# Optimization experiments

Hardware: AMD Instinct MI355X
Metric: run time of the kernel (lower is better)

## Reference

```python
import jax, jax.numpy as jnp
import numpy as np

VOCAB, EMB, HID, B, S = 32000, 256, 512, 64, 512


def setup_inputs() -> dict:
    key = jax.random.key(0)
    ks = jax.random.split(key, 8)
    sc = 0.05
    return {
        "X": jax.random.randint(ks[0], (B, S), 0, VOCAB, dtype=jnp.int32),
        "emb": jax.random.normal(ks[1], (VOCAB, EMB), jnp.float32) * sc,
        "W_ih": jax.random.normal(ks[2], (HID, EMB), jnp.float32) * sc,
        "W_hh": jax.random.normal(ks[3], (HID, HID), jnp.float32) * sc,
        "b_ih": jax.random.normal(ks[4], (HID,), jnp.float32) * sc,
        "b_hh": jax.random.normal(ks[5], (HID,), jnp.float32) * sc,
        "W": jax.random.normal(ks[6], (VOCAB, 2 * HID), jnp.float32) * sc,
        "b": jnp.ones((VOCAB,), jnp.float32),
    }


def reference(X, emb, W_ih, W_hh, b_ih, b_hh, W, b):
    # Embedding lookup -> [S, B, E] (seq-first, like torch RNN default)
    x = emb[X].transpose(1, 0, 2)
    # Precompute input projections for all steps: [S, B, H]
    xin = jnp.einsum('sbe,he->sbh', x, W_ih) + b_ih + b_hh
    h0 = jnp.zeros((X.shape[0], W_hh.shape[0]), x.dtype)

    def step(h, xt):
        h = jnp.tanh(xt + h @ W_hh.T)
        return h, h

    _, outputs = jax.lax.scan(step, h0, xin)  # [S, B, H]
    last = outputs[-1]                         # [B, H]
    prev = outputs[:-1]                        # [S-1, B, H]
    # Attention scores between each previous step and the last output
    scores = jnp.einsum('sbh,bh->sb', prev, last)      # [S-1, B]
    attn = jax.nn.softmax(scores, axis=0)              # softmax over time
    ctx = jnp.einsum('sb,sbh->bh', attn, prev)         # [B, H]
    feat = jnp.concatenate([ctx, last], axis=1)        # [B, 2H]
    return feat @ W.T + b                              # [B, n_class]
```

## Files before the change

kernel.cpp:

```cpp
#include <hip/hip_runtime.h>
#include <hip/hip_fp16.h>
#include <stdint.h>

#define VOCAB 32000
#define EMB   256
#define HID   512
#define BATCH 64
#define SEQ   512

typedef _Float16 h2_t __attribute__((ext_vector_type(2)));

__device__ __forceinline__ float fdot2(unsigned int a, unsigned int b, float c) {
#if __has_builtin(__builtin_amdgcn_fdot2)
    return __builtin_amdgcn_fdot2(__builtin_bit_cast(h2_t, a),
                                  __builtin_bit_cast(h2_t, b), c, false);
#else
    __half2 ah = __builtin_bit_cast(__half2, a);
    __half2 bh = __builtin_bit_cast(__half2, b);
    float2 af = __half22float2(ah), bf = __half22float2(bh);
    return fmaf(af.y, bf.y, fmaf(af.x, bf.x, c));
#endif
}

template<int CTRL>
__device__ __forceinline__ float quad_add(float x) {
    int v = __builtin_amdgcn_update_dpp(0, __builtin_bit_cast(int, x),
                                        CTRL, 0xF, 0xF, true);
    return x + __builtin_bit_cast(float, v);
}
__device__ __forceinline__ float quad_reduce(float x) {
    x = quad_add<0xB1>(x);
    x = quad_add<0x4E>(x);
    return x;
}

__global__ void prep_whh(const float* __restrict__ W_hh, unsigned int* __restrict__ Wpk) {
    int idx = blockIdx.x * blockDim.x + threadIdx.x;
    if (idx >= HID * (HID / 2)) return;
    int r = idx & (HID - 1);
    int j = idx >> 9;
    float lo = W_hh[r * HID + 2 * j];
    float hi = W_hh[r * HID + 2 * j + 1];
    unsigned int u = ((unsigned int)__half_as_ushort(__float2half(hi)) << 16)
                   |  (unsigned int)__half_as_ushort(__float2half(lo));
    Wpk[idx] = u;
}

#define TSA 132

__global__ __launch_bounds__(256) void embed_gemm(
    const int* __restrict__ X, const float* __restrict__ emb,
    const float* __restrict__ W_ih, const float* __restrict__ b_ih,
    const float* __restrict__ b_hh, __half* __restrict__ xin) {
    __shared__ float A_l[32 * TSA];
    __shared__ float B_l[32 * TSA];
    const int tid = threadIdx.x;
    const int tx = tid & 15, ty = tid >> 4;
    const int sb0 = blockIdx.x * 128;
    const int h0  = blockIdx.y * 128;

    float acc[8][8] = {};

    for (int kc = 0; kc < EMB; kc += 32) {
#pragma unroll
        for (int q = 0; q < 4; ++q) {
            int idx = q * 256 + tid;
            int r  = idx >> 3;
            int c4 = idx & 7;
            int row = X[sb0 + r];
            float4 v = *(const float4*)(emb + (size_t)row * EMB + kc + c4 * 4);
            A_l[(c4 * 4 + 0) * TSA + r] = v.x;
            A_l[(c4 * 4 + 1) * TSA + r] = v.y;
            A_l[(c4 * 4 + 2) * TSA + r] = v.z;
            A_l[(c4 * 4 + 3) * TSA + r] = v.w;
        }
#pragma unroll
        for (int q = 0; q < 4; ++q) {
            int idx = q * 256 + tid;
            int r  = idx >> 3;
            int c4 = idx & 7;
            float4 v = *(const float4*)(W_ih + (size_t)(h0 + r) * EMB + kc + c4 * 4);
            B_l[(c4 * 4 + 0) * TSA + r] = v.x;
            B_l[(c4 * 4 + 1) * TSA + r] = v.y;
            B_l[(c4 * 4 + 2) * TSA + r] = v.z;
            B_l[(c4 * 4 + 3) * TSA + r] = v.w;
        }
        __syncthreads();
#pragma unroll
        for (int k = 0; k < 32; ++k) {
            float4 a0 = *(const float4*)&A_l[k * TSA + ty * 4];
            float4 a1 = *(const float4*)&A_l[k * TSA + 64 + ty * 4];
            float4 b0 = *(const float4*)&B_l[k * TSA + tx * 4];
            float4 b1 = *(const float4*)&B_l[k * TSA + 64 + tx * 4];
            float ar[8] = {a0.x, a0.y, a0.z, a0.w, a1.x, a1.y, a1.z, a1.w};
            float br[8] = {b0.x, b0.y, b0.z, b0.w, b1.x, b1.y, b1.z, b1.w};
#pragma unroll
            for (int i = 0; i < 8; ++i)
#pragma unroll
                for (int j = 0; j < 8; ++j)
                    acc[i][j] = fmaf(ar[i], br[j], acc[i][j]);
        }
        __syncthreads();
    }

    float bias[8];
#pragma unroll
    for (int j = 0; j < 8; ++j) {
        int h = h0 + (j < 4 ? tx * 4 + j : 64 + tx * 4 + (j - 4));
        bias[j] = b_ih[h] + b_hh[h];
    }
#pragma unroll
    for (int i = 0; i < 8; ++i) {
        int r = sb0 + (i < 4 ? ty * 4 + i : 64 + ty * 4 + (i - 4));
        __half* dst = xin + (size_t)r * HID + h0;
        __half2 v01 = __floats2half2_rn(acc[i][0] + bias[0], acc[i][1] + bias[1]);
        __half2 v23 = __floats2half2_rn(acc[i][2] + bias[2], acc[i][3] + bias[3]);
        __half2 v45 = __floats2half2_rn(acc[i][4] + bias[4], acc[i][5] + bias[5]);
        __half2 v67 = __floats2half2_rn(acc[i][6] + bias[6], acc[i][7] + bias[7]);
        *(__half2*)(dst + tx * 4)          = v01;
        *(__half2*)(dst + tx * 4 + 2)      = v23;
        *(__half2*)(dst + 64 + tx * 4)     = v45;
        *(__half2*)(dst + 64 + tx * 4 + 2) = v67;
    }
}

#define QSTRIDE 272
#define HBUF_DW 272
#define NREG    56
#define NTAIL   8
#define WT_STR  36

__global__
__attribute__((amdgpu_flat_work_group_size(512, 512), amdgpu_waves_per_eu(2, 2)))
void rnn_scan(
    __half* __restrict__ buf,
    const unsigned int* __restrict__ Wpk) {
    __shared__ unsigned int wt[WT_STR * 512];
    __shared__ unsigned int hbuf[2 * HBUF_DW];

    const int t = threadIdx.x;
    const int b = blockIdx.x;
    const int g = t & 3;
    const int p = t >> 2;

    unsigned int wreg[4 * NREG];
#pragma unroll
    for (int i = 0; i < 4; ++i)
#pragma unroll
        for (int off = 0; off < NREG; ++off)
            wreg[i * NREG + off] = Wpk[(g * 64 + off) * HID + p + 128 * i];
#pragma unroll
    for (int k = 0; k < NTAIL; ++k)
#pragma unroll
        for (int i = 0; i < 4; ++i)
            wt[t * WT_STR + k * 4 + i] = Wpk[(g * 64 + NREG + k) * HID + p + 128 * i];
    for (int i = t; i < 2 * HBUF_DW; i += 512) hbuf[i] = 0;
    __syncthreads();

    const int rf = p + 128 * g;
    const __half* xp = buf + (size_t)b * SEQ * HID + rf;
    __half* op = buf + (size_t)b * SEQ * HID + rf;
    const uint4* wt4 = (const uint4*)&wt[t * WT_STR];

    float xcur = __half2float(xp[0]);
    __half hprev = __float2half(0.0f);

    for (int s = 0; s < SEQ; ++s) {
        if (s > 0) op[(size_t)(s - 1) * HID] = hprev;
        float xnext = 0.0f;
        if (s + 1 < SEQ) xnext = __half2float(xp[(size_t)(s + 1) * HID]);

        const uint4* hq = (const uint4*)((const char*)hbuf
                              + (s & 1) * (HBUF_DW * 4) + g * QSTRIDE);
        float acc[4] = {0.f, 0.f, 0.f, 0.f};
#pragma unroll
        for (int q = 0; q < 14; ++q) {
            uint4 h4 = hq[q];
#pragma unroll
            for (int i = 0; i < 4; ++i) {
                const unsigned int* wi = &wreg[i * NREG + 4 * q];
                acc[i] = fdot2(wi[0], h4.x, acc[i]);
                acc[i] = fdot2(wi[1], h4.y, acc[i]);
                acc[i] = fdot2(wi[2], h4.z, acc[i]);
                acc[i] = fdot2(wi[3], h4.w, acc[i]);
            }
        }
        {
            uint4 h14 = hq[14];
            uint4 h15 = hq[15];
            unsigned int hc[NTAIL] = {h14.x, h14.y, h14.z, h14.w,
                                      h15.x, h15.y, h15.z, h15.w};
#pragma unroll
            for (int k = 0; k < NTAIL; ++k) {
                uint4 w = wt4[k];
                acc[0] = fdot2(w.x, hc[k], acc[0]);
                acc[1] = fdot2(w.y, hc[k], acc[1]);
                acc[2] = fdot2(w.z, hc[k], acc[2]);
                acc[3] = fdot2(w.w, hc[k], acc[3]);
            }
        }
        acc[0] = quad_reduce(acc[0]);
        acc[1] = quad_reduce(acc[1]);
        acc[2] = quad_reduce(acc[2]);
        acc[3] = quad_reduce(acc[3]);
        float dot = (g & 2) ? ((g & 1) ? acc[3] : acc[2])
                            : ((g & 1) ? acc[1] : acc[0]);
        float z = xcur + dot;
        float e = __expf(2.0f * z);
        float hn = 1.0f - 2.0f / (e + 1.0f);
        __half hh = __float2half(hn);
        *((__half*)((char*)hbuf + ((s + 1) & 1) * (HBUF_DW * 4) + g * QSTRIDE) + p) = hh;
        hprev = hh;
        xcur = xnext;
        __syncthreads();
    }
    op[(size_t)(SEQ - 1) * HID] = hprev;
}

__global__ __launch_bounds__(256) void attn_ctx(
    const __half* __restrict__ h_all, float* __restrict__ feat) {
    const int b = blockIdx.x, tid = threadIdx.x;
    __shared__ float lastv[HID];
    __shared__ float sc[SEQ];
    __shared__ float red[256];
    const __half* hb = h_all + (size_t)b * SEQ * HID;

    for (int i = tid; i < HID; i += 256)
        lastv[i] = __half2float(hb[(size_t)(SEQ - 1) * HID + i]);
    __syncthreads();

    for (int s = tid; s < SEQ - 1; s += 256) {
        const __half* row = hb + (size_t)s * HID;
        float acc = 0.f;
        for (int r = 0; r < HID; r += 2) {
            __half2 hv = *(const __half2*)(row + r);
            float2 f = __half22float2(hv);
            acc = fmaf(f.x, lastv[r], acc);
            acc = fmaf(f.y, lastv[r + 1], acc);
        }
        sc[s] = acc;
    }
    __syncthreads();

    float m = -1e30f;
    for (int s = tid; s < SEQ - 1; s += 256) m = fmaxf(m, sc[s]);
    red[tid] = m;
    __syncthreads();
    for (int o = 128; o > 0; o >>= 1) {
        if (tid < o) red[tid] = fmaxf(red[tid], red[tid + o]);
        __syncthreads();
    }
    m = red[0];
    __syncthreads();

    float psum = 0.f;
    for (int s = tid; s < SEQ - 1; s += 256) {
        float e = expf(sc[s] - m);
        sc[s] = e;
        psum += e;
    }
    red[tid] = psum;
    __syncthreads();
    for (int o = 128; o > 0; o >>= 1) {
        if (tid < o) red[tid] += red[tid + o];
        __syncthreads();
    }
    float inv = 1.0f / red[0];
    __syncthreads();

    for (int r2 = tid; r2 < HID / 2; r2 += 256) {
        int r = r2 * 2;
        float accx = 0.f, accy = 0.f;
        int s = 0;
        for (; s + 4 <= SEQ - 1; s += 4) {
#pragma unroll
            for (int u = 0; u < 4; ++u) {
                __half2 hv = *(const __half2*)(hb + (size_t)(s + u) * HID + r);
                float2 f = __half22float2(hv);
                float w = sc[s + u];
                accx = fmaf(w, f.x, accx);
                accy = fmaf(w, f.y, accy);
            }
        }
        for (; s < SEQ - 1; ++s) {
            __half2 hv = *(const __half2*)(hb + (size_t)s * HID + r);
            float2 f = __half22float2(hv);
            float w = sc[s];
            accx = fmaf(w, f.x, accx);
            accy = fmaf(w, f.y, accy);
        }
        feat[(size_t)b * 2 * HID + r]     = accx * inv;
        feat[(size_t)b * 2 * HID + r + 1] = accy * inv;
        feat[(size_t)b * 2 * HID + HID + r]     = lastv[r];
        feat[(size_t)b * 2 * HID + HID + r + 1] = lastv[r + 1];
    }
}

#define TS 68

__global__ __launch_bounds__(256) void final_gemm(
    const float* __restrict__ W, const float* __restrict__ bias,
    const float* __restrict__ feat, float* __restrict__ out) {
    __shared__ float A_l[64 * TS];
    __shared__ float B_l[64 * TS];
    const int tid = threadIdx.x;
    const int tx = tid & 15, ty = tid >> 4;
    const int v0 = blockIdx.x * 64;

    float acc[4][4] = {};

    for (int kc = 0; kc < 2 * HID; kc += 64) {
#pragma unroll
        for (int q = 0; q < 4; ++q) {
            int idx = q * 256 + tid;
            int r  = idx >> 4;
            int c4 = idx & 15;
            const float4 v = *(const float4*)(W + (size_t)(v0 + r) * (2 * HID) + kc + c4 * 4);
            A_l[(c4 * 4 + 0) * TS + r] = v.x;
            A_l[(c4 * 4 + 1) * TS + r] = v.y;
            A_l[(c4 * 4 + 2) * TS + r] = v.z;
            A_l[(c4 * 4 + 3) * TS + r] = v.w;
        }
#pragma unroll
        for (int q = 0; q < 4; ++q) {
            int idx = q * 256 + tid;
            int r  = idx >> 4;
            int c4 = idx & 15;
            const float4 v = *(const float4*)(feat + (size_t)r * (2 * HID) + kc + c4 * 4);
            B_l[(c4 * 4 + 0) * TS + r] = v.x;
            B_l[(c4 * 4 + 1) * TS + r] = v.y;
            B_l[(c4 * 4 + 2) * TS + r] = v.z;
            B_l[(c4 * 4 + 3) * TS + r] = v.w;
        }
        __syncthreads();
#pragma unroll 8
        for (int k = 0; k < 64; ++k) {
            float4 av = *(const float4*)&A_l[k * TS + ty * 4];
            float4 bv = *(const float4*)&B_l[k * TS + tx * 4];
            float a[4] = {av.x, av.y, av.z, av.w};
            float bb[4] = {bv.x, bv.y, bv.z, bv.w};
#pragma unroll
            for (int i = 0; i < 4; ++i)
#pragma unroll
                for (int ii = 0; ii < 4; ++ii)
                    acc[i][ii] = fmaf(a[i], bb[ii], acc[i][ii]);
        }
        __syncthreads();
    }

    float bs[4];
#pragma unroll
    for (int i = 0; i < 4; ++i) bs[i] = bias[v0 + ty * 4 + i];
#pragma unroll
    for (int ii = 0; ii < 4; ++ii) {
        int bb = tx * 4 + ii;
        float4 o;
        o.x = acc[0][ii] + bs[0];
        o.y = acc[1][ii] + bs[1];
        o.z = acc[2][ii] + bs[2];
        o.w = acc[3][ii] + bs[3];
        *(float4*)(out + (size_t)bb * VOCAB + v0 + ty * 4) = o;
    }
}

extern "C" void kernel_launch(void* const* d_in, const int* in_sizes, int n_in,
                              void* d_out, int out_size, void* d_ws, size_t ws_size,
                              hipStream_t stream) {
    const int*   X    = (const int*)d_in[0];
    const float* emb  = (const float*)d_in[1];
    const float* W_ih = (const float*)d_in[2];
    const float* W_hh = (const float*)d_in[3];
    const float* b_ih = (const float*)d_in[4];
    const float* b_hh = (const float*)d_in[5];
    const float* W    = (const float*)d_in[6];
    const float* bias = (const float*)d_in[7];
    float* out = (float*)d_out;

    const size_t BUF_B  = (size_t)BATCH * SEQ * HID * sizeof(__half);
    const size_t WPK_B  = (size_t)(HID * HID / 2) * sizeof(unsigned);
    const size_t FEAT_B = (size_t)BATCH * 2 * HID * sizeof(float);
    if (ws_size < BUF_B + WPK_B + FEAT_B) return;

    char* ws = (char*)d_ws;
    __half*       buf  = (__half*)ws;
    unsigned int* Wpk  = (unsigned int*)(ws + BUF_B);
    float*        feat = (float*)(ws + BUF_B + WPK_B);

    prep_whh<<<(HID * HID / 2 + 255) / 256, 256, 0, stream>>>(W_hh, Wpk);
    embed_gemm<<<dim3(BATCH * SEQ / 128, HID / 128), 256, 0, stream>>>(
        X, emb, W_ih, b_ih, b_hh, buf);
    rnn_scan<<<BATCH, 512, 0, stream>>>(buf, Wpk);
    attn_ctx<<<BATCH, 256, 0, stream>>>(buf, feat);
    final_gemm<<<VOCAB / 64, 256, 0, stream>>>(W, bias, feat, out);
}
```

Baseline: 1.054 ms.

## Use MFMA 16x16x32 f16 for recurrent matvec in RNN scan

Replaces the per-thread fdot2 matvec in the recurrent scan with MFMA 16x16x32 f16 instructions. W_hh is repacked into MFMA A-fragment tiles, 48 tiles held in registers and 16 in LDS. The h vector occupies only one column of B; other lanes read zeros. Results go through an LDS reduction buffer, which adds a second barrier per step, and most of each MFMA's work is wasted on padding columns.

```diff
diff --git a/kernel.cpp b/kernel.cpp
--- a/kernel.cpp
+++ b/kernel.cpp
@@ -8,42 +8,32 @@
 #define BATCH 64
 #define SEQ   512
 
-typedef _Float16 h2_t __attribute__((ext_vector_type(2)));
-
-__device__ __forceinline__ float fdot2(unsigned int a, unsigned int b, float c) {
-#if __has_builtin(__builtin_amdgcn_fdot2)
-    return __builtin_amdgcn_fdot2(__builtin_bit_cast(h2_t, a),
-                                  __builtin_bit_cast(h2_t, b), c, false);
-#else
-    __half2 ah = __builtin_bit_cast(__half2, a);
-    __half2 bh = __builtin_bit_cast(__half2, b);
-    float2 af = __half22float2(ah), bf = __half22float2(bh);
-    return fmaf(af.y, bf.y, fmaf(af.x, bf.x, c));
-#endif
-}
-
-template<int CTRL>
-__device__ __forceinline__ float quad_add(float x) {
-    int v = __builtin_amdgcn_update_dpp(0, __builtin_bit_cast(int, x),
-                                        CTRL, 0xF, 0xF, true);
-    return x + __builtin_bit_cast(float, v);
-}
-__device__ __forceinline__ float quad_reduce(float x) {
-    x = quad_add<0xB1>(x);
-    x = quad_add<0x4E>(x);
-    return x;
-}
-
-__global__ void prep_whh(const float* __restrict__ W_hh, unsigned int* __restrict__ Wpk) {
-    int idx = blockIdx.x * blockDim.x + threadIdx.x;
-    if (idx >= HID * (HID / 2)) return;
-    int r = idx & (HID - 1);
-    int j = idx >> 9;
-    float lo = W_hh[r * HID + 2 * j];
-    float hi = W_hh[r * HID + 2 * j + 1];
-    unsigned int u = ((unsigned int)__half_as_ushort(__float2half(hi)) << 16)
-                   |  (unsigned int)__half_as_ushort(__float2half(lo));
-    Wpk[idx] = u;
+typedef _Float16 f16x8 __attribute__((ext_vector_type(8)));
+typedef float    f32x4 __attribute__((ext_vector_type(4)));
+
+__device__ __forceinline__ unsigned int pack2(float x, float y) {
+    __half2 h = __floats2half2_rn(x, y);
+    return __builtin_bit_cast(unsigned int, h);
+}
+
+__global__ void prep_whh(const float* __restrict__ W_hh, uint4* __restrict__ Apk) {
+    int gid = blockIdx.x * blockDim.x + threadIdx.x;
+    if (gid >= 64 * 512) return;
+    int t    = gid & 511;
+    int tile = gid >> 9;
+    int w = t >> 6, l = t & 63;
+    int ks = tile >> 2, rtl = tile & 3;
+    int m  = (w * 4 + rtl) * 16 + (l & 15);
+    int kb = ks * 32 + (l >> 4) * 8;
+    const float* src = W_hh + (size_t)m * HID + kb;
+    float4 v0 = *(const float4*)(src);
+    float4 v1 = *(const float4*)(src + 4);
+    uint4 o;
+    o.x = pack2(v0.x, v0.y);
+    o.y = pack2(v0.z, v0.w);
+    o.z = pack2(v1.x, v1.y);
+    o.w = pack2(v1.z, v1.w);
+    Apk[(size_t)tile * 512 + t] = o;
 }
 
 #define TSA 132
@@ -124,92 +114,88 @@
     }
 }
 
-#define QSTRIDE 272
-#define HBUF_DW 272
-#define NREG    56
-#define NTAIL   8
-#define WT_STR  36
+#define NRF 48
+#define NLT 16
 
 __global__
 __attribute__((amdgpu_flat_work_group_size(512, 512), amdgpu_waves_per_eu(2, 2)))
 void rnn_scan(
     __half* __restrict__ buf,
-    const unsigned int* __restrict__ Wpk) {
-    __shared__ unsigned int wt[WT_STR * 512];
-    __shared__ unsigned int hbuf[2 * HBUF_DW];
+    const uint4* __restrict__ Apk) {
+    __shared__ uint4  wt[512 * 17];
+    __shared__ __half hbuf[2][HID];
+    __shared__ float  dred[HID];
+    __shared__ float  zp[4];
 
     const int t = threadIdx.x;
     const int b = blockIdx.x;
-    const int g = t & 3;
-    const int p = t >> 2;
-
-    unsigned int wreg[4 * NREG];
-#pragma unroll
-    for (int i = 0; i < 4; ++i)
-#pragma unroll
-        for (int off = 0; off < NREG; ++off)
-            wreg[i * NREG + off] = Wpk[(g * 64 + off) * HID + p + 128 * i];
-#pragma unroll
-    for (int k = 0; k < NTAIL; ++k)
-#pragma unroll
-        for (int i = 0; i < 4; ++i)
-            wt[t * WT_STR + k * 4 + i] = Wpk[(g * 64 + NREG + k) * HID + p + 128 * i];
-    for (int i = t; i < 2 * HBUF_DW; i += 512) hbuf[i] = 0;
-    __syncthreads();
-
-    const int rf = p + 128 * g;
-    const __half* xp = buf + (size_t)b * SEQ * HID + rf;
-    __half* op = buf + (size_t)b * SEQ * HID + rf;
-    const uint4* wt4 = (const uint4*)&wt[t * WT_STR];
+    const int l = t & 63;
+    const int w = t >> 6;
+    const int q = l >> 4;
+    const bool act = (l & 15) == 0;
+
+    f16x8 wreg[NRF];
+#pragma unroll
+    for (int i = 0; i < NRF; ++i)
+        wreg[i] = __builtin_bit_cast(f16x8, Apk[(size_t)i * 512 + t]);
+#pragma unroll
+    for (int i = 0; i < NLT; ++i)
+        wt[t * 17 + i] = Apk[(size_t)(NRF + i) * 512 + t];
+    for (int i = t; i < 2 * HID; i += 512) ((__half*)hbuf)[i] = __float2half(0.0f);
+    if (t < 4) zp[t] = 0.0f;
+    __syncthreads();
+
+    const __half* xp = buf + (size_t)b * SEQ * HID + t;
+    __half*       op = buf + (size_t)b * SEQ * HID + t;
 
     float xcur = __half2float(xp[0]);
     __half hprev = __float2half(0.0f);
+
+    const char* hb_base = (const char*)hbuf;
+    const char* zpp     = (const char*)zp;
+    const int   bstride = act ? 64 : 0;
 
     for (int s = 0; s < SEQ; ++s) {
         if (s > 0) op[(size_t)(s - 1) * HID] = hprev;
         float xnext = 0.0f;
         if (s + 1 < SEQ) xnext = __half2float(xp[(size_t)(s + 1) * HID]);
 
-        const uint4* hq = (const uint4*)((const char*)hbuf
-                              + (s & 1) * (HBUF_DW * 4) + g * QSTRIDE);
-        float acc[4] = {0.f, 0.f, 0.f, 0.f};
-#pragma unroll
-        for (int q = 0; q < 14; ++q) {
-            uint4 h4 = hq[q];
-#pragma unroll
-            for (int i = 0; i < 4; ++i) {
-                const unsigned int* wi = &wreg[i * NREG + 4 * q];
-                acc[i] = fdot2(wi[0], h4.x, acc[i]);
-                acc[i] = fdot2(wi[1], h4.y, acc[i]);
-                acc[i] = fdot2(wi[2], h4.z, acc[i]);
-                acc[i] = fdot2(wi[3], h4.w, acc[i]);
+        const char* bp = act ? (hb_base + (s & 1) * (HID * 2) + q * 16) : zpp;
+
+        f32x4 acc[4] = {};
+#pragma unroll
+        for (int ks = 0; ks < 12; ++ks) {
+            f16x8 bf = *(const f16x8*)bp;
+            bp += bstride;
+#pragma unroll
+            for (int rtl = 0; rtl < 4; ++rtl)
+                acc[rtl] = __builtin_amdgcn_mfma_f32_16x16x32_f16(
+                    wreg[ks * 4 + rtl], bf, acc[rtl], 0, 0, 0);
+        }
+#pragma unroll
+        for (int ks = 12; ks < 16; ++ks) {
+            f16x8 bf = *(const f16x8*)bp;
+            bp += bstride;
+#pragma unroll
+            for (int rtl = 0; rtl < 4; ++rtl) {
+                f16x8 af = __builtin_bit_cast(f16x8, wt[t * 17 + (ks - 12) * 4 + rtl]);
+                acc[rtl] = __builtin_amdgcn_mfma_f32_16x16x32_f16(
+                    af, bf, acc[rtl], 0, 0, 0);
             }
         }
-        {
-            uint4 h14 = hq[14];
-            uint4 h15 = hq[15];
-            unsigned int hc[NTAIL] = {h14.x, h14.y, h14.z, h14.w,
-                                      h15.x, h15.y, h15.z, h15.w};
-#pragma unroll
-            for (int k = 0; k < NTAIL; ++k) {
-                uint4 w = wt4[k];
-                acc[0] = fdot2(w.x, hc[k], acc[0]);
-                acc[1] = fdot2(w.y, hc[k], acc[1]);
-                acc[2] = fdot2(w.z, hc[k], acc[2]);
-                acc[3] = fdot2(w.w, hc[k], acc[3]);
-            }
-        }
-        acc[0] = quad_reduce(acc[0]);
-        acc[1] = quad_reduce(acc[1]);
-        acc[2] = quad_reduce(acc[2]);
-        acc[3] = quad_reduce(acc[3]);
-        float dot = (g & 2) ? ((g & 1) ? acc[3] : acc[2])
-                            : ((g & 1) ? acc[1] : acc[0]);
-        float z = xcur + dot;
+
+        if (act) {
+#pragma unroll
+            for (int rtl = 0; rtl < 4; ++rtl)
+                *(f32x4*)&dred[w * 64 + rtl * 16 + q * 4] = acc[rtl];
+        }
+        __syncthreads();
+
+        float z = xcur + dred[t];
         float e = __expf(2.0f * z);
         float hn = 1.0f - 2.0f / (e + 1.0f);
         __half hh = __float2half(hn);
-        *((__half*)((char*)hbuf + ((s + 1) & 1) * (HBUF_DW * 4) + g * QSTRIDE) + p) = hh;
+        hbuf[(s + 1) & 1][t] = hh;
         hprev = hh;
         xcur = xnext;
         __syncthreads();
@@ -377,19 +363,19 @@
     float* out = (float*)d_out;
 
     const size_t BUF_B  = (size_t)BATCH * SEQ * HID * sizeof(__half);
-    const size_t WPK_B  = (size_t)(HID * HID / 2) * sizeof(unsigned);
+    const size_t APK_B  = (size_t)64 * 512 * sizeof(uint4);
     const size_t FEAT_B = (size_t)BATCH * 2 * HID * sizeof(float);
-    if (ws_size < BUF_B + WPK_B + FEAT_B) return;
+    if (ws_size < BUF_B + APK_B + FEAT_B) return;
 
     char* ws = (char*)d_ws;
-    __half*       buf  = (__half*)ws;
-    unsigned int* Wpk  = (unsigned int*)(ws + BUF_B);
-    float*        feat = (float*)(ws + BUF_B + WPK_B);
-
-    prep_whh<<<(HID * HID / 2 + 255) / 256, 256, 0, stream>>>(W_hh, Wpk);
+    __half* buf  = (__half*)ws;
+    uint4*  Apk  = (uint4*)(ws + BUF_B);
+    float*  feat = (float*)(ws + BUF_B + APK_B);
+
+    prep_whh<<<(64 * 512 + 255) / 256, 256, 0, stream>>>(W_hh, Apk);
     embed_gemm<<<dim3(BATCH * SEQ / 128, HID / 128), 256, 0, stream>>>(
         X, emb, W_ih, b_ih, b_hh, buf);
-    rnn_scan<<<BATCH, 512, 0, stream>>>(buf, Wpk);
+    rnn_scan<<<BATCH, 512, 0, stream>>>(buf, Apk);
     attn_ctx<<<BATCH, 256, 0, stream>>>(buf, feat);
     final_gemm<<<VOCAB / 64, 256, 0, stream>>>(W, bias, feat, out);
 }
```

Result: slower. 1.154 ms (+9.5%).
